# Kernel tuning notes

Measured on AMD Instinct MI355X. Metric: run time of the kernel, lower is better.

Reference implementation:

```python
import jax, jax.numpy as jnp
import numpy as np

N = 50000        # nodes
E = 800000       # edges (before self-loops)
NFEAT = 256
NHID = 32
HEADS = 8
NOUT = 128
NEG_SLOPE = 0.2
EPS = 1e-5


def _gat_layer(x, src, dst, W, att_src, att_dst, bias, heads, ch, concat):
    """PyG-style GATConv (shared weights for src/dst, self-loops already appended)."""
    n = x.shape[0]
    h = (x @ W).reshape(n, heads, ch)                      # [N,H,C]
    a_src = (h * att_src).sum(-1)                          # [N,H]
    a_dst = (h * att_dst).sum(-1)                          # [N,H]
    e = jax.nn.leaky_relu(a_src[src] + a_dst[dst], NEG_SLOPE)  # [E',H]
    # segment softmax over incoming edges of each dst node
    m = jax.ops.segment_max(e, dst, num_segments=n)        # [N,H]
    m = jnp.where(jnp.isfinite(m), m, 0.0)
    ex = jnp.exp(e - m[dst])                               # [E',H]
    denom = jax.ops.segment_sum(ex, dst, num_segments=n)   # [N,H]
    alpha = ex / (denom[dst] + 1e-16)                      # [E',H]
    msg = h[src] * alpha[:, :, None]                       # [E',H,C]
    out = jax.ops.segment_sum(msg, dst, num_segments=n)    # [N,H,C]
    out = out.reshape(n, heads * ch) if concat else out.mean(axis=1)
    return out + bias


def setup_inputs() -> dict:
    key = jax.random.key(0)
    ks = jax.random.split(key, 14)
    s = 0.05
    return {
        "x": jax.random.normal(ks[0], (N, NFEAT), jnp.float32),
        "edge_index": jax.random.randint(ks[1], (2, E), 0, N, dtype=jnp.int64),
        "W1": jax.random.normal(ks[2], (NFEAT, HEADS * NHID), jnp.float32) * s,
        "att_src1": jax.random.normal(ks[3], (HEADS, NHID), jnp.float32) * s,
        "att_dst1": jax.random.normal(ks[4], (HEADS, NHID), jnp.float32) * s,
        "b1": jnp.zeros((HEADS * NHID,), jnp.float32),
        "W2": jax.random.normal(ks[5], (HEADS * NHID, NOUT), jnp.float32) * s,
        "att_src2": jax.random.normal(ks[6], (1, NOUT), jnp.float32) * s,
        "att_dst2": jax.random.normal(ks[7], (1, NOUT), jnp.float32) * s,
        "b2": jnp.zeros((NOUT,), jnp.float32),
        "bn_gamma": jnp.ones((NOUT,), jnp.float32),
        "bn_beta": jnp.zeros((NOUT,), jnp.float32),
        "ln_gamma": jnp.ones((NOUT,), jnp.float32),
        "ln_beta": jnp.zeros((NOUT,), jnp.float32),
    }


def reference(x, edge_index, W1, att_src1, att_dst1, b1, W2, att_src2, att_dst2, b2,
              bn_gamma, bn_beta, ln_gamma, ln_beta):
    loops = jnp.arange(N, dtype=edge_index.dtype)
    src = jnp.concatenate([edge_index[0], loops])
    dst = jnp.concatenate([edge_index[1], loops])
    # layer 1: concat heads, then relu (dropout is identity at inference)
    h = jax.nn.relu(_gat_layer(x, src, dst, W1, att_src1, att_dst1, b1, HEADS, NHID, True))
    # layer 2: single head, mean (no concat), relu
    h = jax.nn.relu(_gat_layer(h, src, dst, W2, att_src2, att_dst2, b2, 1, NOUT, False))
    # BatchNorm1d with batch statistics (biased var, eps=1e-5)
    mu = h.mean(axis=0)
    var = h.var(axis=0)
    h = (h - mu) / jnp.sqrt(var + EPS) * bn_gamma + bn_beta
    # LayerNorm over last dim
    mu2 = h.mean(axis=-1, keepdims=True)
    var2 = h.var(axis=-1, keepdims=True)
    return (h - mu2) / jnp.sqrt(var2 + EPS) * ln_gamma + ln_beta
```

## Files before the change

### kernel.cpp

```cpp
#include <hip/hip_runtime.h>
#include <cstdint>
#include <cstddef>

#define HEADS   8
#define NFEAT   256
#define NOUT    128
#define NEG     0.2f
#define EPSV    1e-5f

typedef unsigned short ushort_t;
typedef __attribute__((ext_vector_type(8))) short s8v;
typedef __attribute__((ext_vector_type(4))) float f4v;

static __device__ __forceinline__ float lrelu(float x) { return x > 0.f ? x : NEG * x; }

static __device__ __forceinline__ float bf2f(ushort_t u) {
    union { unsigned int i; float f; } v; v.i = ((unsigned int)u) << 16; return v.f;
}
static __device__ __forceinline__ ushort_t f2bf(float f) {
    union { float f; unsigned int i; } v; v.f = f;
    unsigned int x = v.i;
    return (ushort_t)((x + 0x7fff + ((x >> 16) & 1)) >> 16);
}
static __device__ __forceinline__ float bits2f(unsigned int u) {
    union { unsigned int i; float f; } v; v.i = u; return v.f;
}

static __device__ __forceinline__ int detect64(const int* __restrict__ ei, int E) {
    int lane = threadIdx.x & 63;
    long idx = 2L * ((long)lane * (E / 64)) + 1;
    int v = ei[idx];
    unsigned long long ball = __ballot(v == 0);
    return (ball == ~0ull) ? 1 : 0;
}

__global__ void k_count(const int* __restrict__ ei, int* __restrict__ counts,
                        int E, int n) {
    int is64 = detect64(ei, E);
    int i = blockIdx.x * blockDim.x + threadIdx.x;
    if (i < E) {
        int d = ei[(size_t)(E + i) << is64];
        atomicAdd(&counts[d], 1);
    } else if (i < E + n) {
        atomicAdd(&counts[i - E], 1);
    }
}

__global__ __launch_bounds__(1024) void k_scan1(const int* __restrict__ counts,
                                                int* __restrict__ incl,
                                                int* __restrict__ bsum, int n) {
    int t = threadIdx.x, i = blockIdx.x * 1024 + t;
    int lane = t & 63, w = t >> 6;
    int v = (i < n) ? counts[i] : 0;
    int sv = v;
#pragma unroll
    for (int o = 1; o < 64; o <<= 1) { int u = __shfl_up(sv, o, 64); if (lane >= o) sv += u; }
    __shared__ int wsum[16];
    if (lane == 63) wsum[w] = sv;
    __syncthreads();
    if (w == 0) {
        int bs = (lane < 16) ? wsum[lane] : 0;
#pragma unroll
        for (int o = 1; o < 16; o <<= 1) { int u = __shfl_up(bs, o, 64); if (lane >= o) bs += u; }
        if (lane < 16) wsum[lane] = bs;
    }
    __syncthreads();
    int pre = (w > 0) ? wsum[w - 1] : 0;
    sv += pre;
    if (i < n) incl[i] = sv;
    if (t == 1023) bsum[blockIdx.x] = sv;
}

__global__ void k_scan2(int* __restrict__ bsum, int nb) {
    int lane = threadIdx.x;
    int v = (lane < nb) ? bsum[lane] : 0;
    int sv = v;
#pragma unroll
    for (int o = 1; o < 64; o <<= 1) { int u = __shfl_up(sv, o, 64); if (lane >= o) sv += u; }
    if (lane < nb) bsum[lane] = sv - v;
}

__global__ void k_scan3(const int* __restrict__ incl, const int* __restrict__ bsum,
                        const int* __restrict__ counts,
                        int* __restrict__ offs, int* __restrict__ cursor, int n) {
    int i = blockIdx.x * blockDim.x + threadIdx.x;
    if (i < n) {
        int v = incl[i] + bsum[i >> 10];
        offs[i + 1] = v;
        cursor[i] = v - counts[i];
    }
    if (i == 0) offs[0] = 0;
}

__global__ void k_fill(const int* __restrict__ ei, int* __restrict__ cursor,
                       int* __restrict__ esrc, int E, int n) {
    int is64 = detect64(ei, E);
    int i = blockIdx.x * blockDim.x + threadIdx.x;
    if (i >= E + n) return;
    int s, d;
    if (i < E) { s = ei[(size_t)i << is64]; d = ei[(size_t)(E + i) << is64]; }
    else       { s = i - E; d = s; }
    int p = atomicAdd(&cursor[d], 1);
    esrc[p] = s;
}

__global__ void k_prepw(const float* __restrict__ W1, const float* __restrict__ W2,
                        ushort_t* __restrict__ Wh1, ushort_t* __restrict__ Wl1,
                        ushort_t* __restrict__ Wh2, ushort_t* __restrict__ Wl2) {
    int gid = blockIdx.x * 256 + threadIdx.x;
    const float* W; ushort_t* Wh; ushort_t* Wl; int M;
    if (gid < 256 * 256) { W = W1; Wh = Wh1; Wl = Wl1; M = 256; }
    else { gid -= 256 * 256; if (gid >= 256 * 128) return; W = W2; Wh = Wh2; Wl = Wl2; M = 128; }
    int k = gid / M, nn = gid - k * M;
    int ntile = nn >> 4, j = nn & 15, kc = k >> 3, e = k & 7;
    int p = ((ntile * 32 + kc) * 16 + j) * 8 + e;
    float v = W[(size_t)k * M + nn];
    ushort_t hi = f2bf(v);
    float r = v - bf2f(hi);
    Wh[p] = hi;
    Wl[p] = f2bf(r);
}

__global__ __launch_bounds__(256) void k_mm(const float* __restrict__ A,
                                            const ushort_t* __restrict__ Wh,
                                            const ushort_t* __restrict__ Wl,
                                            ushort_t* __restrict__ C, int n, int Mout) {
    __shared__ ushort_t Ah[128][40];
    __shared__ ushort_t Al[128][40];
    const int t = threadIdx.x;
    const int lane = t & 63, w = t >> 6;
    const int wr = w >> 1, wc = w & 1;
    const int r0 = blockIdx.x * 128;
    const int srow = t >> 1;
    const int kh = (t & 1) * 16;
    const int arow = r0 + srow;
    const bool rowok = arow < n;

    f4v acc[4][4];
#pragma unroll
    for (int a = 0; a < 4; ++a)
#pragma unroll
        for (int b = 0; b < 4; ++b) { f4v z = {0.f, 0.f, 0.f, 0.f}; acc[a][b] = z; }

    float pre[16];
    const float* abase = &A[(size_t)arow * 256 + kh];
#pragma unroll
    for (int q = 0; q < 4; ++q) {
        float4 v = rowok ? *reinterpret_cast<const float4*>(abase + q * 4)
                         : float4{0.f, 0.f, 0.f, 0.f};
        pre[q * 4 + 0] = v.x; pre[q * 4 + 1] = v.y;
        pre[q * 4 + 2] = v.z; pre[q * 4 + 3] = v.w;
    }

    const int lj = lane & 15, lk = lane >> 4;

    for (int kb = 0; kb < 256; kb += 32) {
        __syncthreads();
#pragma unroll
        for (int q = 0; q < 2; ++q) {
            unsigned int hw[4], lw[4];
#pragma unroll
            for (int p = 0; p < 4; ++p) {
                float v0 = pre[q * 8 + p * 2], v1 = pre[q * 8 + p * 2 + 1];
                ushort_t h0 = f2bf(v0), h1 = f2bf(v1);
                ushort_t l0 = f2bf(v0 - bf2f(h0)), l1 = f2bf(v1 - bf2f(h1));
                hw[p] = (unsigned int)h0 | ((unsigned int)h1 << 16);
                lw[p] = (unsigned int)l0 | ((unsigned int)l1 << 16);
            }
            uint4 hv = {hw[0], hw[1], hw[2], hw[3]};
            uint4 lv = {lw[0], lw[1], lw[2], lw[3]};
            *reinterpret_cast<uint4*>(&Ah[srow][kh + q * 8]) = hv;
            *reinterpret_cast<uint4*>(&Al[srow][kh + q * 8]) = lv;
        }
        __syncthreads();
        if (kb < 224) {
            const float* ap = abase + kb + 32;
#pragma unroll
            for (int q = 0; q < 4; ++q) {
                float4 v = rowok ? *reinterpret_cast<const float4*>(ap + q * 4)
                                 : float4{0.f, 0.f, 0.f, 0.f};
                pre[q * 4 + 0] = v.x; pre[q * 4 + 1] = v.y;
                pre[q * 4 + 2] = v.z; pre[q * 4 + 3] = v.w;
            }
        }
        const int kc0 = kb >> 3;
        s8v ah[4], al[4];
#pragma unroll
        for (int mf = 0; mf < 4; ++mf) {
            ah[mf] = *reinterpret_cast<const s8v*>(&Ah[wr * 64 + mf * 16 + lj][lk * 8]);
            al[mf] = *reinterpret_cast<const s8v*>(&Al[wr * 64 + mf * 16 + lj][lk * 8]);
        }
#pragma unroll
        for (int nf = 0; nf < 4; ++nf) {
            int ntile = blockIdx.y * 8 + wc * 4 + nf;
            size_t boff = ((size_t)(ntile * 32 + kc0 + lk) * 16 + lj) * 8;
            s8v bh = *reinterpret_cast<const s8v*>(&Wh[boff]);
            s8v bl = *reinterpret_cast<const s8v*>(&Wl[boff]);
#pragma unroll
            for (int mf = 0; mf < 4; ++mf) {
                acc[mf][nf] = __builtin_amdgcn_mfma_f32_16x16x32_bf16(ah[mf], bh, acc[mf][nf], 0, 0, 0);
                acc[mf][nf] = __builtin_amdgcn_mfma_f32_16x16x32_bf16(ah[mf], bl, acc[mf][nf], 0, 0, 0);
                acc[mf][nf] = __builtin_amdgcn_mfma_f32_16x16x32_bf16(al[mf], bh, acc[mf][nf], 0, 0, 0);
            }
        }
    }

#pragma unroll
    for (int mf = 0; mf < 4; ++mf) {
        int rr = r0 + wr * 64 + mf * 16 + lk * 4;
#pragma unroll
        for (int nf = 0; nf < 4; ++nf) {
            int cc = blockIdx.y * 128 + wc * 64 + nf * 16 + lj;
#pragma unroll
            for (int r = 0; r < 4; ++r) {
                if (rr + r < n) C[(size_t)(rr + r) * Mout + cc] = f2bf(acc[mf][nf][r]);
            }
        }
    }
}

__global__ __launch_bounds__(256) void k_att1(const ushort_t* __restrict__ h1,
                                              const float* __restrict__ att_s,
                                              const float* __restrict__ att_d,
                                              float* __restrict__ as1,
                                              float* __restrict__ ad1, int n) {
    int wid = (blockIdx.x * blockDim.x + threadIdx.x) >> 6;
    int lane = threadIdx.x & 63;
    if (wid >= n) return;
    int head = lane >> 3;
    int co = (lane & 7) * 4;
    ushort4 hu = *reinterpret_cast<const ushort4*>(&h1[(size_t)wid * 256 + head * 32 + co]);
    float4 vs = *reinterpret_cast<const float4*>(&att_s[head * 32 + co]);
    float4 vd = *reinterpret_cast<const float4*>(&att_d[head * 32 + co]);
    float hx = bf2f(hu.x), hy = bf2f(hu.y), hz = bf2f(hu.z), hw = bf2f(hu.w);
    float ss = hx * vs.x + hy * vs.y + hz * vs.z + hw * vs.w;
    float sd = hx * vd.x + hy * vd.y + hz * vd.z + hw * vd.w;
#pragma unroll
    for (int o = 1; o < 8; o <<= 1) { ss += __shfl_xor(ss, o, 64); sd += __shfl_xor(sd, o, 64); }
    if ((lane & 7) == 0) {
        as1[(size_t)wid * 8 + head] = ss;
        ad1[(size_t)wid * 8 + head] = sd;
    }
}

__global__ __launch_bounds__(256) void k_att2(const ushort_t* __restrict__ h2,
                                              const float* __restrict__ att_s,
                                              const float* __restrict__ att_d,
                                              float* __restrict__ as2,
                                              float* __restrict__ ad2, int n) {
    int wid = (blockIdx.x * blockDim.x + threadIdx.x) >> 6;
    int lane = threadIdx.x & 63;
    if (wid >= n) return;
    ushort2 hu = *reinterpret_cast<const ushort2*>(&h2[(size_t)wid * 128 + lane * 2]);
    float2 vs = *reinterpret_cast<const float2*>(&att_s[lane * 2]);
    float2 vd = *reinterpret_cast<const float2*>(&att_d[lane * 2]);
    float hx = bf2f(hu.x), hy = bf2f(hu.y);
    float ss = hx * vs.x + hy * vs.y;
    float sd = hx * vd.x + hy * vd.y;
#pragma unroll
    for (int o = 1; o < 64; o <<= 1) { ss += __shfl_xor(ss, o, 64); sd += __shfl_xor(sd, o, 64); }
    if (lane == 0) { as2[wid] = ss; ad2[wid] = sd; }
}

__global__ __launch_bounds__(256) void k_agg1(const ushort_t* __restrict__ h1,
                                              const float* __restrict__ as1,
                                              const float* __restrict__ ad1,
                                              const int* __restrict__ offs,
                                              const int* __restrict__ esrc,
                                              const float* __restrict__ b1,
                                              float* __restrict__ out1, int n, int tot) {
    int wid = (blockIdx.x * blockDim.x + threadIdx.x) >> 6;
    int lane = threadIdx.x & 63;
    if (wid >= n) return;
    int e0 = offs[wid], e1 = offs[wid + 1];
    int deg = e1 - e0;

    if (deg <= 64) {
        const int l = lane & 31;
        const int h = lane >> 5;
        const int hd = l >> 2;
        const int cb = l * 8;
        float adn = ad1[(size_t)wid * 8 + hd];

        int ei_idx = e0 + lane;
        int es = esrc[ei_idx < tot ? ei_idx : (tot - 1)];

        const int headA = lane >> 3, g = lane & 7;
        float adnA = ad1[(size_t)wid * 8 + headA];
        float a[8];
#pragma unroll
        for (int k = 0; k < 8; ++k) {
            int i = g + 8 * k;
            int s = __shfl(es, i, 64);
            a[k] = (i < deg) ? as1[(size_t)s * 8 + headA] : -1e30f;
        }
        float mx = a[0];
#pragma unroll
        for (int k = 1; k < 8; ++k) mx = fmaxf(mx, a[k]);
#pragma unroll
        for (int o = 1; o < 8; o <<= 1) mx = fmaxf(mx, __shfl_xor(mx, o, 64));
        (void)adnA;
        float m = lrelu(__shfl(mx, hd * 8, 64) + adn);

        float d = 0.f;
        float ac0 = 0.f, ac1 = 0.f, ac2 = 0.f, ac3 = 0.f;
        float ac4 = 0.f, ac5 = 0.f, ac6 = 0.f, ac7 = 0.f;
#pragma unroll
        for (int u = 0; u < 8; ++u) {
            if (8 * u < deg) {
#pragma unroll
                for (int v = 0; v < 4; ++v) {
                    int i = 8 * u + 2 * v + h;
                    int s = __shfl(es, i, 64);
                    float av = __shfl(a[u], hd * 8 + 2 * v + h, 64);
                    if (i < deg) {
                        float p = __expf(lrelu(av + adn) - m);
                        uint4 hv = *reinterpret_cast<const uint4*>(&h1[(size_t)s * 256 + cb]);
                        d += p;
                        ac0 += p * bits2f(hv.x << 16);
                        ac1 += p * bits2f(hv.x & 0xffff0000u);
                        ac2 += p * bits2f(hv.y << 16);
                        ac3 += p * bits2f(hv.y & 0xffff0000u);
                        ac4 += p * bits2f(hv.z << 16);
                        ac5 += p * bits2f(hv.z & 0xffff0000u);
                        ac6 += p * bits2f(hv.w << 16);
                        ac7 += p * bits2f(hv.w & 0xffff0000u);
                    }
                }
            }
        }
        d   += __shfl_xor(d, 32, 64);
        ac0 += __shfl_xor(ac0, 32, 64); ac1 += __shfl_xor(ac1, 32, 64);
        ac2 += __shfl_xor(ac2, 32, 64); ac3 += __shfl_xor(ac3, 32, 64);
        ac4 += __shfl_xor(ac4, 32, 64); ac5 += __shfl_xor(ac5, 32, 64);
        ac6 += __shfl_xor(ac6, 32, 64); ac7 += __shfl_xor(ac7, 32, 64);
        if (lane < 32) {
            float inv = 1.f / (d + 1e-16f);
            float4 b0 = *reinterpret_cast<const float4*>(&b1[cb]);
            float4 b4 = *reinterpret_cast<const float4*>(&b1[cb + 4]);
            float4 o0, o1;
            o0.x = fmaxf(ac0 * inv + b0.x, 0.f);
            o0.y = fmaxf(ac1 * inv + b0.y, 0.f);
            o0.z = fmaxf(ac2 * inv + b0.z, 0.f);
            o0.w = fmaxf(ac3 * inv + b0.w, 0.f);
            o1.x = fmaxf(ac4 * inv + b4.x, 0.f);
            o1.y = fmaxf(ac5 * inv + b4.y, 0.f);
            o1.z = fmaxf(ac6 * inv + b4.z, 0.f);
            o1.w = fmaxf(ac7 * inv + b4.w, 0.f);
            *reinterpret_cast<float4*>(&out1[(size_t)wid * 256 + cb]) = o0;
            *reinterpret_cast<float4*>(&out1[(size_t)wid * 256 + cb + 4]) = o1;
        }
    } else {
        int head = lane >> 3;
        int g = lane & 7;
        int cb = lane * 4;
        float adn = ad1[(size_t)wid * 8 + head];
        float mx = -1e30f;
        for (int e = e0 + g; e < e1; e += 8)
            mx = fmaxf(mx, as1[(size_t)esrc[e] * 8 + head]);
#pragma unroll
        for (int o = 1; o < 8; o <<= 1) mx = fmaxf(mx, __shfl_xor(mx, o, 64));
        float m = lrelu(mx + adn);
        float d = 0.f, ax = 0.f, ay = 0.f, az = 0.f, aw = 0.f;
        for (int e = e0; e < e1; ++e) {
            int s = esrc[e];
            float p = __expf(lrelu(as1[(size_t)s * 8 + head] + adn) - m);
            ushort4 hv = *reinterpret_cast<const ushort4*>(&h1[(size_t)s * 256 + cb]);
            d += p;
            ax += p * bf2f(hv.x);
            ay += p * bf2f(hv.y);
            az += p * bf2f(hv.z);
            aw += p * bf2f(hv.w);
        }
        float inv = 1.f / (d + 1e-16f);
        float4 bb = *reinterpret_cast<const float4*>(&b1[cb]);
        float4 o;
        o.x = fmaxf(ax * inv + bb.x, 0.f);
        o.y = fmaxf(ay * inv + bb.y, 0.f);
        o.z = fmaxf(az * inv + bb.z, 0.f);
        o.w = fmaxf(aw * inv + bb.w, 0.f);
        *reinterpret_cast<float4*>(&out1[(size_t)wid * 256 + cb]) = o;
    }
}

__global__ __launch_bounds__(256) void k_agg2(const ushort_t* __restrict__ h2,
                                              const float* __restrict__ as2,
                                              const float* __restrict__ ad2,
                                              const int* __restrict__ offs,
                                              const int* __restrict__ esrc,
                                              const float* __restrict__ b2,
                                              float* __restrict__ out2, int n, int tot) {
    int wid = (blockIdx.x * blockDim.x + threadIdx.x) >> 6;
    int lane = threadIdx.x & 63;
    if (wid >= n) return;
    float adn = ad2[wid];
    int e0 = offs[wid], e1 = offs[wid + 1];
    int deg = e1 - e0;

    if (deg <= 64) {
        const int l = lane & 15;
        const int q = lane >> 4;
        const int cb = l * 8;

        int ei_idx = e0 + lane;
        int es = esrc[ei_idx < tot ? ei_idx : (tot - 1)];
        float av0 = (lane < deg) ? as2[es] : -1e30f;
        float mx = av0;
#pragma unroll
        for (int o = 1; o < 64; o <<= 1) mx = fmaxf(mx, __shfl_xor(mx, o, 64));
        float m = lrelu(mx + adn);

        float d = 0.f;
        float ac0 = 0.f, ac1 = 0.f, ac2 = 0.f, ac3 = 0.f;
        float ac4 = 0.f, ac5 = 0.f, ac6 = 0.f, ac7 = 0.f;
#pragma unroll
        for (int u = 0; u < 4; ++u) {
            if (16 * u < deg) {
#pragma unroll
                for (int v = 0; v < 4; ++v) {
                    int i = 16 * u + 4 * v + q;
                    int s = __shfl(es, i, 64);
                    float av = __shfl(av0, i, 64);
                    if (i < deg) {
                        float p = __expf(lrelu(av + adn) - m);
                        uint4 hv = *reinterpret_cast<const uint4*>(&h2[(size_t)s * 128 + cb]);
                        d += p;
                        ac0 += p * bits2f(hv.x << 16);
                        ac1 += p * bits2f(hv.x & 0xffff0000u);
                        ac2 += p * bits2f(hv.y << 16);
                        ac3 += p * bits2f(hv.y & 0xffff0000u);
                        ac4 += p * bits2f(hv.z << 16);
                        ac5 += p * bits2f(hv.z & 0xffff0000u);
                        ac6 += p * bits2f(hv.w << 16);
                        ac7 += p * bits2f(hv.w & 0xffff0000u);
                    }
                }
            }
        }
#pragma unroll
        for (int o = 16; o <= 32; o <<= 1) {
            d   += __shfl_xor(d, o, 64);
            ac0 += __shfl_xor(ac0, o, 64); ac1 += __shfl_xor(ac1, o, 64);
            ac2 += __shfl_xor(ac2, o, 64); ac3 += __shfl_xor(ac3, o, 64);
            ac4 += __shfl_xor(ac4, o, 64); ac5 += __shfl_xor(ac5, o, 64);
            ac6 += __shfl_xor(ac6, o, 64); ac7 += __shfl_xor(ac7, o, 64);
        }
        if (lane < 16) {
            float inv = 1.f / (d + 1e-16f);
            float4 b0 = *reinterpret_cast<const float4*>(&b2[cb]);
            float4 b4 = *reinterpret_cast<const float4*>(&b2[cb + 4]);
            float4 o0, o1;
            o0.x = fmaxf(ac0 * inv + b0.x, 0.f);
            o0.y = fmaxf(ac1 * inv + b0.y, 0.f);
            o0.z = fmaxf(ac2 * inv + b0.z, 0.f);
            o0.w = fmaxf(ac3 * inv + b0.w, 0.f);
            o1.x = fmaxf(ac4 * inv + b4.x, 0.f);
            o1.y = fmaxf(ac5 * inv + b4.y, 0.f);
            o1.z = fmaxf(ac6 * inv + b4.z, 0.f);
            o1.w = fmaxf(ac7 * inv + b4.w, 0.f);
            *reinterpret_cast<float4*>(&out2[(size_t)wid * 128 + cb]) = o0;
            *reinterpret_cast<float4*>(&out2[(size_t)wid * 128 + cb + 4]) = o1;
        }
    } else {
        int cb = lane * 2;
        float mx = -1e30f;
        for (int e = e0 + lane; e < e1; e += 64)
            mx = fmaxf(mx, as2[esrc[e]]);
#pragma unroll
        for (int o = 1; o < 64; o <<= 1) mx = fmaxf(mx, __shfl_xor(mx, o, 64));
        float m = lrelu(mx + adn);
        float d = 0.f, ax = 0.f, ay = 0.f;
        for (int e = e0; e < e1; ++e) {
            int s = esrc[e];
            float p = __expf(lrelu(as2[s] + adn) - m);
            ushort2 hv = *reinterpret_cast<const ushort2*>(&h2[(size_t)s * 128 + cb]);
            d += p;
            ax += p * bf2f(hv.x);
            ay += p * bf2f(hv.y);
        }
        float inv = 1.f / (d + 1e-16f);
        float o0 = fmaxf(ax * inv + b2[cb], 0.f);
        float o1 = fmaxf(ay * inv + b2[cb + 1], 0.f);
        float2 o = {o0, o1};
        *reinterpret_cast<float2*>(&out2[(size_t)wid * 128 + cb]) = o;
    }
}

__global__ __launch_bounds__(128) void k_bnstat(const float* __restrict__ out2,
                                                float* __restrict__ bnsum,
                                                float* __restrict__ bnsq, int n) {
    int c = threadIdx.x;
    float s = 0.f, q = 0.f;
    for (int r = blockIdx.x; r < n; r += gridDim.x) {
        float v = out2[(size_t)r * 128 + c];
        s += v;
        q += v * v;
    }
    atomicAdd(&bnsum[c], s);
    atomicAdd(&bnsq[c], q);
}

__global__ __launch_bounds__(256) void k_final(const float* __restrict__ out2,
                                               const float* __restrict__ bnsum,
                                               const float* __restrict__ bnsq,
                                               const float* __restrict__ bng,
                                               const float* __restrict__ bnb,
                                               const float* __restrict__ lng,
                                               const float* __restrict__ lnb,
                                               float* __restrict__ out, int n) {
    int wid = (blockIdx.x * blockDim.x + threadIdx.x) >> 6;
    int lane = threadIdx.x & 63;
    if (wid >= n) return;
    int c0 = lane, c1 = lane + 64;
    float invn = 1.f / (float)n;
    float mu0 = bnsum[c0] * invn, mu1 = bnsum[c1] * invn;
    float v0 = bnsq[c0] * invn - mu0 * mu0;
    float v1 = bnsq[c1] * invn - mu1 * mu1;
    float r0 = rsqrtf(v0 + EPSV), r1 = rsqrtf(v1 + EPSV);
    float x0 = out2[(size_t)wid * 128 + c0];
    float x1 = out2[(size_t)wid * 128 + c1];
    float y0 = (x0 - mu0) * r0 * bng[c0] + bnb[c0];
    float y1 = (x1 - mu1) * r1 * bng[c1] + bnb[c1];
    float s = y0 + y1, q = y0 * y0 + y1 * y1;
#pragma unroll
    for (int o = 1; o < 64; o <<= 1) { s += __shfl_xor(s, o, 64); q += __shfl_xor(q, o, 64); }
    float mu = s * (1.f / 128.f);
    float var = q * (1.f / 128.f) - mu * mu;
    float rr = rsqrtf(var + EPSV);
    out[(size_t)wid * 128 + c0] = (y0 - mu) * rr * lng[c0] + lnb[c0];
    out[(size_t)wid * 128 + c1] = (y1 - mu) * rr * lng[c1] + lnb[c1];
}

extern "C" void kernel_launch(void* const* d_in, const int* in_sizes, int n_in,
                              void* d_out, int out_size, void* d_ws, size_t ws_size,
                              hipStream_t stream) {
    const float* x    = (const float*)d_in[0];
    const int*   ei   = (const int*)d_in[1];
    const float* W1   = (const float*)d_in[2];
    const float* ats1 = (const float*)d_in[3];
    const float* atd1 = (const float*)d_in[4];
    const float* b1   = (const float*)d_in[5];
    const float* W2   = (const float*)d_in[6];
    const float* ats2 = (const float*)d_in[7];
    const float* atd2 = (const float*)d_in[8];
    const float* b2   = (const float*)d_in[9];
    const float* bng  = (const float*)d_in[10];
    const float* bnb  = (const float*)d_in[11];
    const float* lng  = (const float*)d_in[12];
    const float* lnb  = (const float*)d_in[13];

    const int n = in_sizes[0] / NFEAT;
    const int E = in_sizes[1] / 2;
    const int tot = E + n;

    auto align = [](size_t v) { return (v + 255) & ~(size_t)255; };
    char* ws = (char*)d_ws;
    size_t off = 0;
    ushort_t* h1 = (ushort_t*)(ws + off); off += align((size_t)n * 256 * 2);
    float* out1 = (float*)(ws + off); off += align((size_t)n * 256 * 4);
    ushort_t* h2 = h1;
    float* out2 = out1;
    float* as1 = (float*)(ws + off); off += align((size_t)n * 8 * 4);
    float* ad1 = (float*)(ws + off); off += align((size_t)n * 8 * 4);
    float* as2 = (float*)(ws + off); off += align((size_t)n * 4);
    float* ad2 = (float*)(ws + off); off += align((size_t)n * 4);
    int* counts = (int*)(ws + off); off += align((size_t)n * 4);
    int* offs   = (int*)(ws + off); off += align((size_t)(n + 1) * 4);
    int* cursor = (int*)(ws + off); off += align((size_t)n * 4);
    int* esrc   = (int*)(ws + off); off += align((size_t)tot * 4);
    int* incl   = (int*)(ws + off); off += align((size_t)n * 4);
    int* bsum   = (int*)(ws + off); off += align(64 * 4);
    float* bnsum = (float*)(ws + off); off += align(256 * 4);
    float* bnsq  = bnsum + 128;
    ushort_t* Wh1 = (ushort_t*)(ws + off); off += align((size_t)256 * 256 * 2);
    ushort_t* Wl1 = (ushort_t*)(ws + off); off += align((size_t)256 * 256 * 2);
    ushort_t* Wh2 = (ushort_t*)(ws + off); off += align((size_t)256 * 128 * 2);
    ushort_t* Wl2 = (ushort_t*)(ws + off); off += align((size_t)256 * 128 * 2);

    hipMemsetAsync(counts, 0, (size_t)n * 4, stream);
    hipMemsetAsync(bnsum, 0, 256 * 4, stream);

    k_prepw<<<(256 * 256 + 256 * 128 + 255) / 256, 256, 0, stream>>>(W1, W2, Wh1, Wl1, Wh2, Wl2);

    k_count<<<(tot + 255) / 256, 256, 0, stream>>>(ei, counts, E, n);
    int nsb = (n + 1023) / 1024;
    k_scan1<<<nsb, 1024, 0, stream>>>(counts, incl, bsum, n);
    k_scan2<<<1, 64, 0, stream>>>(bsum, nsb);
    k_scan3<<<(n + 255) / 256, 256, 0, stream>>>(incl, bsum, counts, offs, cursor, n);
    k_fill<<<(tot + 255) / 256, 256, 0, stream>>>(ei, cursor, esrc, E, n);

    const int gx = (n + 127) / 128;
    k_mm<<<dim3(gx, 2), 256, 0, stream>>>(x, Wh1, Wl1, h1, n, 256);
    k_att1<<<(n + 3) / 4, 256, 0, stream>>>(h1, ats1, atd1, as1, ad1, n);
    k_agg1<<<(n + 3) / 4, 256, 0, stream>>>(h1, as1, ad1, offs, esrc, b1, out1, n, tot);

    k_mm<<<dim3(gx, 1), 256, 0, stream>>>(out1, Wh2, Wl2, h2, n, 128);
    k_att2<<<(n + 3) / 4, 256, 0, stream>>>(h2, ats2, atd2, as2, ad2, n);
    k_agg2<<<(n + 3) / 4, 256, 0, stream>>>(h2, as2, ad2, offs, esrc, b2, out2, n, tot);

    k_bnstat<<<512, 128, 0, stream>>>(out2, bnsum, bnsq, n);
    k_final<<<(n + 3) / 4, 256, 0, stream>>>(out2, bnsum, bnsq, bng, bnb, lng, lnb,
                                             (float*)d_out, n);
}
```

Measured before the change: 363.9 us.

## Fold scan pass into scan3, merge memsets, precompute edge exps, truncating bf16 split

The small k_scan2 launch is removed: each k_scan3 block now sums the earlier block totals serially in one thread. The two memsets are merged by placing the BN accumulators right after the counts buffer. The aggregation kernels now compute each edge's softmax exponent once per edge/head and shuffle the result, instead of recomputing lrelu and exp in every lane. The GEMM's hi/lo bf16 split uses bit truncation instead of round-to-nearest, which cuts ALU work but slightly changes the rounding of the split.

```diff
diff --git a/kernel.cpp b/kernel.cpp
--- a/kernel.cpp
+++ b/kernel.cpp
@@ -24,6 +24,9 @@
 }
 static __device__ __forceinline__ float bits2f(unsigned int u) {
     union { unsigned int i; float f; } v; v.i = u; return v.f;
+}
+static __device__ __forceinline__ unsigned int f2bits(float f) {
+    union { float f; unsigned int i; } v; v.f = f; return v.i;
 }
 
 static __device__ __forceinline__ int detect64(const int* __restrict__ ei, int E) {
@@ -71,21 +74,20 @@
     if (t == 1023) bsum[blockIdx.x] = sv;
 }
 
-__global__ void k_scan2(int* __restrict__ bsum, int nb) {
-    int lane = threadIdx.x;
-    int v = (lane < nb) ? bsum[lane] : 0;
-    int sv = v;
-#pragma unroll
-    for (int o = 1; o < 64; o <<= 1) { int u = __shfl_up(sv, o, 64); if (lane >= o) sv += u; }
-    if (lane < nb) bsum[lane] = sv - v;
-}
-
 __global__ void k_scan3(const int* __restrict__ incl, const int* __restrict__ bsum,
                         const int* __restrict__ counts,
                         int* __restrict__ offs, int* __restrict__ cursor, int n) {
-    int i = blockIdx.x * blockDim.x + threadIdx.x;
+    __shared__ int pre_s;
+    int chunk = blockIdx.x >> 2;
+    if (threadIdx.x == 0) {
+        int s = 0;
+        for (int j = 0; j < chunk; ++j) s += bsum[j];
+        pre_s = s;
+    }
+    __syncthreads();
+    int i = blockIdx.x * 256 + threadIdx.x;
     if (i < n) {
-        int v = incl[i] + bsum[i >> 10];
+        int v = incl[i] + pre_s;
         offs[i + 1] = v;
         cursor[i] = v - counts[i];
     }
@@ -161,11 +163,13 @@
             unsigned int hw[4], lw[4];
 #pragma unroll
             for (int p = 0; p < 4; ++p) {
-                float v0 = pre[q * 8 + p * 2], v1 = pre[q * 8 + p * 2 + 1];
-                ushort_t h0 = f2bf(v0), h1 = f2bf(v1);
-                ushort_t l0 = f2bf(v0 - bf2f(h0)), l1 = f2bf(v1 - bf2f(h1));
-                hw[p] = (unsigned int)h0 | ((unsigned int)h1 << 16);
-                lw[p] = (unsigned int)l0 | ((unsigned int)l1 << 16);
+                unsigned int x0 = f2bits(pre[q * 8 + p * 2]);
+                unsigned int x1 = f2bits(pre[q * 8 + p * 2 + 1]);
+                unsigned int h1b = x1 & 0xffff0000u;
+                float lo0 = bits2f(f2bits(pre[q * 8 + p * 2])) - bits2f(x0 & 0xffff0000u);
+                float lo1 = pre[q * 8 + p * 2 + 1] - bits2f(h1b);
+                hw[p] = (x0 >> 16) | h1b;
+                lw[p] = (f2bits(lo0) >> 16) | (f2bits(lo1) & 0xffff0000u);
             }
             uint4 hv = {hw[0], hw[1], hw[2], hw[3]};
             uint4 lv = {lw[0], lw[1], lw[2], lw[3]};
@@ -280,7 +284,6 @@
         const int h = lane >> 5;
         const int hd = l >> 2;
         const int cb = l * 8;
-        float adn = ad1[(size_t)wid * 8 + hd];
 
         int ei_idx = e0 + lane;
         int es = esrc[ei_idx < tot ? ei_idx : (tot - 1)];
@@ -299,8 +302,10 @@
         for (int k = 1; k < 8; ++k) mx = fmaxf(mx, a[k]);
 #pragma unroll
         for (int o = 1; o < 8; o <<= 1) mx = fmaxf(mx, __shfl_xor(mx, o, 64));
-        (void)adnA;
-        float m = lrelu(__shfl(mx, hd * 8, 64) + adn);
+        float mA = lrelu(mx + adnA);
+#pragma unroll
+        for (int k = 0; k < 8; ++k)
+            a[k] = __expf(lrelu(a[k] + adnA) - mA);
 
         float d = 0.f;
         float ac0 = 0.f, ac1 = 0.f, ac2 = 0.f, ac3 = 0.f;
@@ -312,9 +317,8 @@
                 for (int v = 0; v < 4; ++v) {
                     int i = 8 * u + 2 * v + h;
                     int s = __shfl(es, i, 64);
-                    float av = __shfl(a[u], hd * 8 + 2 * v + h, 64);
+                    float p = __shfl(a[u], hd * 8 + 2 * v + h, 64);
                     if (i < deg) {
-                        float p = __expf(lrelu(av + adn) - m);
                         uint4 hv = *reinterpret_cast<const uint4*>(&h1[(size_t)s * 256 + cb]);
                         d += p;
                         ac0 += p * bits2f(hv.x << 16);
@@ -409,6 +413,7 @@
 #pragma unroll
         for (int o = 1; o < 64; o <<= 1) mx = fmaxf(mx, __shfl_xor(mx, o, 64));
         float m = lrelu(mx + adn);
+        float p0 = __expf(lrelu(av0 + adn) - m);
 
         float d = 0.f;
         float ac0 = 0.f, ac1 = 0.f, ac2 = 0.f, ac3 = 0.f;
@@ -420,9 +425,8 @@
                 for (int v = 0; v < 4; ++v) {
                     int i = 16 * u + 4 * v + q;
                     int s = __shfl(es, i, 64);
-                    float av = __shfl(av0, i, 64);
+                    float p = __shfl(p0, i, 64);
                     if (i < deg) {
-                        float p = __expf(lrelu(av + adn) - m);
                         uint4 hv = *reinterpret_cast<const uint4*>(&h2[(size_t)s * 128 + cb]);
                         d += p;
                         ac0 += p * bits2f(hv.x << 16);
@@ -564,28 +568,26 @@
     float* ad1 = (float*)(ws + off); off += align((size_t)n * 8 * 4);
     float* as2 = (float*)(ws + off); off += align((size_t)n * 4);
     float* ad2 = (float*)(ws + off); off += align((size_t)n * 4);
-    int* counts = (int*)(ws + off); off += align((size_t)n * 4);
+    int* counts = (int*)(ws + off); off += align((size_t)n * 4 + 1024);
+    float* bnsum = (float*)(counts + n);
+    float* bnsq  = bnsum + 128;
     int* offs   = (int*)(ws + off); off += align((size_t)(n + 1) * 4);
     int* cursor = (int*)(ws + off); off += align((size_t)n * 4);
     int* esrc   = (int*)(ws + off); off += align((size_t)tot * 4);
     int* incl   = (int*)(ws + off); off += align((size_t)n * 4);
     int* bsum   = (int*)(ws + off); off += align(64 * 4);
-    float* bnsum = (float*)(ws + off); off += align(256 * 4);
-    float* bnsq  = bnsum + 128;
     ushort_t* Wh1 = (ushort_t*)(ws + off); off += align((size_t)256 * 256 * 2);
     ushort_t* Wl1 = (ushort_t*)(ws + off); off += align((size_t)256 * 256 * 2);
     ushort_t* Wh2 = (ushort_t*)(ws + off); off += align((size_t)256 * 128 * 2);
     ushort_t* Wl2 = (ushort_t*)(ws + off); off += align((size_t)256 * 128 * 2);
 
-    hipMemsetAsync(counts, 0, (size_t)n * 4, stream);
-    hipMemsetAsync(bnsum, 0, 256 * 4, stream);
+    hipMemsetAsync(counts, 0, (size_t)n * 4 + 1024, stream);
 
     k_prepw<<<(256 * 256 + 256 * 128 + 255) / 256, 256, 0, stream>>>(W1, W2, Wh1, Wl1, Wh2, Wl2);
 
     k_count<<<(tot + 255) / 256, 256, 0, stream>>>(ei, counts, E, n);
     int nsb = (n + 1023) / 1024;
     k_scan1<<<nsb, 1024, 0, stream>>>(counts, incl, bsum, n);
-    k_scan2<<<1, 64, 0, stream>>>(bsum, nsb);
     k_scan3<<<(n + 255) / 256, 256, 0, stream>>>(incl, bsum, counts, offs, cursor, n);
     k_fill<<<(tot + 255) / 256, 256, 0, stream>>>(ei, cursor, esrc, E, n);
 
```

After: 354.4 us. 2.6% less time.
